# Performance work log

Hardware: AMD Instinct MI355X
Metric: run time of the kernel (lower is better)

The kernel has to match this reference:

```python
import jax, jax.numpy as jnp
import numpy as np

N = 50000   # nodes
K = 8       # fixed in-degree per node (edges sorted by target)
NQ = 400000 # quadruplets
TWO_PI = 2.0 * np.pi


def setup_inputs() -> dict:
    key = jax.random.key(0)
    k1, k2 = jax.random.split(key)
    pos = jax.random.normal(k1, (N, 3), dtype=jnp.float32) * 3.0
    # ring-structured graph: node i receives edges from (i+1..i+K) mod N.
    # Edges sorted by target i with exactly K per node -> edges into node n
    # occupy slots [n*K, n*K+K). Since N > 2K, a node is never its own
    # 2-hop self (idx_i != idx_k always holds, matching torch's mask).
    i = np.repeat(np.arange(N, dtype=np.int32), K)
    d = np.tile(np.arange(1, K + 1, dtype=np.int32), N)
    j = (i + d) % N
    edge_index = jnp.asarray(np.stack([j, i]), dtype=jnp.int32)  # [2, E]
    q_index = jax.random.randint(k2, (4, NQ), 0, N, dtype=jnp.int32)
    return {"pos": pos, "edge_index": edge_index, "q_index": q_index}


def _geometry(pos, edge_index, q_index):
    j, i = edge_index[0], edge_index[1]
    E = j.shape[0]

    rel = pos[i] - pos[j]
    dist = jnp.sqrt(jnp.sum(rel * rel, axis=-1))                 # [E]

    # ---- triplets: for edge e=(j->i), k ranges over in-neighbors of j ----
    ar = jnp.arange(K, dtype=j.dtype)
    idx_kj = (j[:, None] * K + ar[None, :]).reshape(-1)          # [T] edge ids k->j
    idx_ji = jnp.repeat(jnp.arange(E, dtype=j.dtype), K)         # [T] edge ids j->i
    idx_i = i[idx_ji]
    idx_j = j[idx_ji]
    idx_k = j[idx_kj]

    pos_ji = pos[idx_i] - pos[idx_j]                             # [T,3]
    pos_jk = pos[idx_k] - pos[idx_j]                             # [T,3]
    a = jnp.sum(pos_ji * pos_jk, axis=-1)
    b = jnp.linalg.norm(jnp.cross(pos_ji, pos_jk), axis=-1)
    angle = jnp.arctan2(b, a)                                    # [T]

    # ---- quadruplets: k_n ranges over the K in-neighbors of idx_j ----
    kn_edges = idx_j[:, None] * K + ar[None, :]                  # [T,K]
    idx_k_n = j[kn_edges]                                        # [T,K]
    pos_jkn = pos[idx_k_n] - pos[idx_j][:, None, :]              # [T,K,3]
    plane1 = jnp.cross(pos_ji, pos_jk)                           # [T,3]
    plane2 = jnp.cross(pos_ji[:, None, :], pos_jkn)              # [T,K,3]
    dist_ji = jnp.sqrt(jnp.sum(pos_ji * pos_ji, axis=-1))        # [T]
    a2 = jnp.sum(plane1[:, None, :] * plane2, axis=-1)           # [T,K]
    b2 = jnp.sum(jnp.cross(plane1[:, None, :], plane2) * pos_ji[:, None, :], axis=-1) / dist_ji[:, None]
    torsion = jnp.arctan2(b2, a2)
    torsion = jnp.where(torsion <= 0, torsion + TWO_PI, torsion)
    valid = (idx_k_n != idx_i[:, None]) & (idx_k_n != idx_k[:, None])
    # scatter_min over quadruplets grouped by triplet == masked row-min
    torsiona = jnp.min(jnp.where(valid, torsion, jnp.inf), axis=-1)  # [T]

    plane_s = 0.5 * jnp.sin(angle) * dist[idx_kj] * dist[idx_ji]     # [T]

    # ---- tetrahedron volumes for quadruplets q_index [4,NQ] ----
    pq = pos[q_index.T]                                          # [NQ,4,3]
    v1 = pq[:, 1] - pq[:, 0]
    v2 = pq[:, 2] - pq[:, 0]
    v3 = pq[:, 3] - pq[:, 0]
    volume = jnp.abs(jnp.sum(jnp.cross(v1, v2) * v3, axis=-1)) / 6.0  # [NQ]

    return dist, angle, torsiona, plane_s, volume, idx_ji, idx_kj


def reference(pos, edge_index, q_index):
    dist, angle, torsiona, plane_s, volume, idx_ji, idx_kj = _geometry(pos, edge_index, q_index)
    # matches torch return: (dist, angle, torsiona, torsiona, torsiona, plane_s, volume, idx_ji, idx_kj)
    return (dist, angle, torsiona, torsiona, torsiona, plane_s, volume, idx_ji, idx_kj)
```

## Files before the change

### kernel.cpp

```cpp
#include <hip/hip_runtime.h>

#define KDEG 8
constexpr float TWO_PI_F = 6.28318530717958647692f;
constexpr float PI_F = 3.14159265358979323846f;
constexpr float PI_2_F = 1.57079632679489661923f;
constexpr float MIN_SENTINEL = 1000.0f;

struct F3 { float x, y, z; };
__device__ __forceinline__ F3 f3sub(F3 a, F3 b) { return {a.x - b.x, a.y - b.y, a.z - b.z}; }
__device__ __forceinline__ float f3dot(F3 a, F3 b) { return a.x * b.x + a.y * b.y + a.z * b.z; }
__device__ __forceinline__ F3 f3cross(F3 a, F3 b) {
  return {a.y * b.z - a.z * b.y, a.z * b.x - a.x * b.z, a.x * b.y - a.y * b.x};
}
__device__ __forceinline__ F3 ldpos(const float* __restrict__ p, int idx) {
  return {p[3 * idx], p[3 * idx + 1], p[3 * idx + 2]};
}

__device__ __forceinline__ float fast_atan01(float z) {
  float z2 = z * z;
  float p = fmaf(z2, 0.0208351f, -0.0851330f);
  p = fmaf(z2, p, 0.1801410f);
  p = fmaf(z2, p, -0.3302995f);
  p = fmaf(z2, p, 0.9998660f);
  return z * p;
}

__device__ __forceinline__ float fast_atan2(float y, float x) {
  float ax = fabsf(x), ay = fabsf(y);
  float mx = fmaxf(ax, ay);
  float mn = fminf(ax, ay);
  float z = mn * __builtin_amdgcn_rcpf(fmaxf(mx, 1e-30f));
  float r = fast_atan01(z);
  r = (ay > ax) ? (PI_2_F - r) : r;
  r = (x < 0.0f) ? (PI_F - r) : r;
  return (y < 0.0f) ? -r : r;
}

__device__ __forceinline__ void edge_work(
    int e,
    const float* __restrict__ pos,
    const int* __restrict__ ei_j,
    const int* __restrict__ ei_i,
    float* __restrict__ out,
    int off_angle, int off_t0, int off_t1, int off_t2,
    int off_ps, int off_iji, int off_ikj)
{
  int j = ei_j[e];
  int i = ei_i[e];
  F3 pj = ldpos(pos, j);
  F3 pi = ldpos(pos, i);
  F3 pji = f3sub(pi, pj);
  float d2 = f3dot(pji, pji);
  float inv_dji = rsqrtf(d2);
  float dji = d2 * inv_dji;
  float inv_d2 = inv_dji * inv_dji;
  out[e] = dji;

  int base = j * KDEG;
  int nbr[KDEG];
#pragma unroll
  for (int n = 0; n < KDEG; n++) nbr[n] = ei_j[base + n];

  F3 u[KDEG], pl[KDEG];
  float s[KDEG], ang[KDEG], hb[KDEG];
#pragma unroll
  for (int n = 0; n < KDEG; n++) {
    u[n] = f3sub(ldpos(pos, nbr[n]), pj);
    s[n] = f3dot(pji, u[n]);
    pl[n] = f3cross(pji, u[n]);
    float b = sqrtf(f3dot(pl[n], pl[n]));
    ang[n] = fast_atan2(b, s[n]);
    hb[n] = 0.5f * b;
  }

  int t0 = e * KDEG;
  float4 v0, v1;
  v0 = {ang[0], ang[1], ang[2], ang[3]};
  v1 = {ang[4], ang[5], ang[6], ang[7]};
  *reinterpret_cast<float4*>(out + off_angle + t0) = v0;
  *reinterpret_cast<float4*>(out + off_angle + t0 + 4) = v1;
  v0 = {hb[0], hb[1], hb[2], hb[3]};
  v1 = {hb[4], hb[5], hb[6], hb[7]};
  *reinterpret_cast<float4*>(out + off_ps + t0) = v0;
  *reinterpret_cast<float4*>(out + off_ps + t0 + 4) = v1;

  bool vi[KDEG];
#pragma unroll
  for (int n = 0; n < KDEG; n++) vi[n] = (nbr[n] != i);

  float mn[KDEG];
#pragma unroll
  for (int n = 0; n < KDEG; n++) mn[n] = MIN_SENTINEL;

#pragma unroll
  for (int kk = 0; kk < KDEG; kk++) {
#pragma unroll
    for (int n = kk + 1; n < KDEG; n++) {
      float m = f3dot(u[kk], u[n]);
      float Traw = f3dot(u[kk], pl[n]);
      float x = fmaf(-s[kk] * s[n], inv_d2, m);
      float y = -Traw * inv_dji;
      float t1 = fast_atan2(y, x);
      float f1 = (t1 <= 0.0f) ? t1 + TWO_PI_F : t1;
      float t2 = -t1;
      float f2 = (t2 <= 0.0f) ? t2 + TWO_PI_F : t2;
      bool same = (nbr[n] == nbr[kk]);
      if (vi[n] && !same) mn[kk] = fminf(mn[kk], f1);
      if (vi[kk] && !same) mn[n] = fminf(mn[n], f2);
    }
  }

  v0 = {mn[0], mn[1], mn[2], mn[3]};
  v1 = {mn[4], mn[5], mn[6], mn[7]};
  *reinterpret_cast<float4*>(out + off_t0 + t0) = v0;
  *reinterpret_cast<float4*>(out + off_t0 + t0 + 4) = v1;
  *reinterpret_cast<float4*>(out + off_t1 + t0) = v0;
  *reinterpret_cast<float4*>(out + off_t1 + t0 + 4) = v1;
  *reinterpret_cast<float4*>(out + off_t2 + t0) = v0;
  *reinterpret_cast<float4*>(out + off_t2 + t0 + 4) = v1;

  float fe = (float)e;
  v0 = {fe, fe, fe, fe};
  *reinterpret_cast<float4*>(out + off_iji + t0) = v0;
  *reinterpret_cast<float4*>(out + off_iji + t0 + 4) = v0;

  float fb = (float)base;
  v0 = {fb, fb + 1.0f, fb + 2.0f, fb + 3.0f};
  v1 = {fb + 4.0f, fb + 5.0f, fb + 6.0f, fb + 7.0f};
  *reinterpret_cast<float4*>(out + off_ikj + t0) = v0;
  *reinterpret_cast<float4*>(out + off_ikj + t0 + 4) = v1;
}

__device__ __forceinline__ void volume_work(
    int t,
    const float* __restrict__ pos,
    const int* __restrict__ q,
    float* __restrict__ out,
    int NQ, int off_vol)
{
  int q0 = q[t];
  int q1 = q[t + NQ];
  int q2 = q[t + 2 * NQ];
  int q3 = q[t + 3 * NQ];
  F3 p0 = ldpos(pos, q0);
  F3 p1 = ldpos(pos, q1);
  F3 p2 = ldpos(pos, q2);
  F3 p3 = ldpos(pos, q3);
  F3 v1 = f3sub(p1, p0);
  F3 v2 = f3sub(p2, p0);
  F3 v3 = f3sub(p3, p0);
  float vol = fabsf(f3dot(f3cross(v1, v2), v3)) * (1.0f / 6.0f);
  out[off_vol + t] = vol;
}

__global__ __launch_bounds__(256) void fused_kernel(
    const float* __restrict__ pos,
    const int* __restrict__ ei_j,
    const int* __restrict__ ei_i,
    const int* __restrict__ q,
    float* __restrict__ out,
    int E, int NQ, int nbE,
    int off_angle, int off_t0, int off_t1, int off_t2,
    int off_ps, int off_vol, int off_iji, int off_ikj)
{
  int b = blockIdx.x;
  if (b < nbE) {
    int e = b * blockDim.x + threadIdx.x;
    if (e < E)
      edge_work(e, pos, ei_j, ei_i, out,
                off_angle, off_t0, off_t1, off_t2, off_ps, off_iji, off_ikj);
  } else {
    int t = (b - nbE) * blockDim.x + threadIdx.x;
    if (t < NQ)
      volume_work(t, pos, q, out, NQ, off_vol);
  }
}

extern "C" void kernel_launch(void* const* d_in, const int* in_sizes, int n_in,
                              void* d_out, int out_size, void* d_ws, size_t ws_size,
                              hipStream_t stream) {
  const float* pos = (const float*)d_in[0];
  const int* edge_index = (const int*)d_in[1];
  const int* q_index = (const int*)d_in[2];

  const int E = in_sizes[1] / 2;
  const int NQ = in_sizes[2] / 4;
  const int T = E * KDEG;

  const int* ei_j = edge_index;
  const int* ei_i = edge_index + E;

  float* out = (float*)d_out;

  const int off_angle = E;
  const int off_t0 = off_angle + T;
  const int off_t1 = off_t0 + T;
  const int off_t2 = off_t1 + T;
  const int off_ps = off_t2 + T;
  const int off_vol = off_ps + T;
  const int off_iji = off_vol + NQ;
  const int off_ikj = off_iji + T;
  (void)out_size; (void)d_ws; (void)ws_size; (void)n_in;

  const int blk = 256;
  const int nbE = (E + blk - 1) / blk;
  const int nbQ = (NQ + blk - 1) / blk;

  fused_kernel<<<nbE + nbQ, blk, 0, stream>>>(
      pos, ei_j, ei_i, q_index, out, E, NQ, nbE,
      off_angle, off_t0, off_t1, off_t2, off_ps, off_vol, off_iji, off_ikj);
}
```

Measured before the change: 33.21 us.

## Compute torsions as azimuth differences in a per-edge orthonormal frame

Builds a fixed perpendicular frame (e1, e2) around each edge direction and projects every neighbor onto it to get one azimuth per neighbor. The pairwise torsion angle then becomes a difference of two azimuths, which replaces the 28 atan2 calls plus dot and cross products in the inner pair loop with subtractions. Fewer live registers (no u/pl arrays) may also help occupancy. The risk is precision loss and wraparound near the ±pi edges of atan2, and a degenerate frame when the edge is parallel to the fixed vector G.

```diff
diff --git a/kernel.cpp b/kernel.cpp
--- a/kernel.cpp
+++ b/kernel.cpp
@@ -53,24 +53,32 @@
   float d2 = f3dot(pji, pji);
   float inv_dji = rsqrtf(d2);
   float dji = d2 * inv_dji;
-  float inv_d2 = inv_dji * inv_dji;
   out[e] = dji;
+
+  const F3 G = {0.53452248f, -0.26726124f, 0.80178373f};
+  F3 e1 = f3cross(pji, G);
+  F3 e2 = f3cross(pji, e1);
+  float L2 = f3dot(e1, e1);
+  float invL = rsqrtf(fmaxf(L2, 1e-30f));
+  float djinvL = dji * invL;
 
   int base = j * KDEG;
   int nbr[KDEG];
 #pragma unroll
   for (int n = 0; n < KDEG; n++) nbr[n] = ei_j[base + n];
 
-  F3 u[KDEG], pl[KDEG];
-  float s[KDEG], ang[KDEG], hb[KDEG];
+  float phi[KDEG], ang[KDEG], hb[KDEG];
 #pragma unroll
   for (int n = 0; n < KDEG; n++) {
-    u[n] = f3sub(ldpos(pos, nbr[n]), pj);
-    s[n] = f3dot(pji, u[n]);
-    pl[n] = f3cross(pji, u[n]);
-    float b = sqrtf(f3dot(pl[n], pl[n]));
-    ang[n] = fast_atan2(b, s[n]);
-    hb[n] = 0.5f * b;
+    F3 u = f3sub(ldpos(pos, nbr[n]), pj);
+    float s = f3dot(pji, u);
+    float a = f3dot(e1, u);
+    float b = f3dot(e2, u) * inv_dji;
+    phi[n] = fast_atan2(b, a);
+    float perp = sqrtf(fmaf(a, a, b * b));
+    float bfull = perp * djinvL;
+    ang[n] = fast_atan2(bfull, s);
+    hb[n] = 0.5f * bfull;
   }
 
   int t0 = e * KDEG;
@@ -84,6 +92,16 @@
   *reinterpret_cast<float4*>(out + off_ps + t0) = v0;
   *reinterpret_cast<float4*>(out + off_ps + t0 + 4) = v1;
 
+  float fe = (float)e;
+  v0 = {fe, fe, fe, fe};
+  *reinterpret_cast<float4*>(out + off_iji + t0) = v0;
+  *reinterpret_cast<float4*>(out + off_iji + t0 + 4) = v0;
+  float fb = (float)base;
+  v0 = {fb, fb + 1.0f, fb + 2.0f, fb + 3.0f};
+  v1 = {fb + 4.0f, fb + 5.0f, fb + 6.0f, fb + 7.0f};
+  *reinterpret_cast<float4*>(out + off_ikj + t0) = v0;
+  *reinterpret_cast<float4*>(out + off_ikj + t0 + 4) = v1;
+
   bool vi[KDEG];
 #pragma unroll
   for (int n = 0; n < KDEG; n++) vi[n] = (nbr[n] != i);
@@ -96,14 +114,10 @@
   for (int kk = 0; kk < KDEG; kk++) {
 #pragma unroll
     for (int n = kk + 1; n < KDEG; n++) {
-      float m = f3dot(u[kk], u[n]);
-      float Traw = f3dot(u[kk], pl[n]);
-      float x = fmaf(-s[kk] * s[n], inv_d2, m);
-      float y = -Traw * inv_dji;
-      float t1 = fast_atan2(y, x);
-      float f1 = (t1 <= 0.0f) ? t1 + TWO_PI_F : t1;
-      float t2 = -t1;
-      float f2 = (t2 <= 0.0f) ? t2 + TWO_PI_F : t2;
+      float d = phi[n] - phi[kk];
+      float f1 = (d <= 0.0f) ? d + TWO_PI_F : d;
+      float f2 = TWO_PI_F - f1;
+      f2 = (f2 <= 0.0f) ? f2 + TWO_PI_F : f2;
       bool same = (nbr[n] == nbr[kk]);
       if (vi[n] && !same) mn[kk] = fminf(mn[kk], f1);
       if (vi[kk] && !same) mn[n] = fminf(mn[n], f2);
@@ -118,17 +132,6 @@
   *reinterpret_cast<float4*>(out + off_t1 + t0 + 4) = v1;
   *reinterpret_cast<float4*>(out + off_t2 + t0) = v0;
   *reinterpret_cast<float4*>(out + off_t2 + t0 + 4) = v1;
-
-  float fe = (float)e;
-  v0 = {fe, fe, fe, fe};
-  *reinterpret_cast<float4*>(out + off_iji + t0) = v0;
-  *reinterpret_cast<float4*>(out + off_iji + t0 + 4) = v0;
-
-  float fb = (float)base;
-  v0 = {fb, fb + 1.0f, fb + 2.0f, fb + 3.0f};
-  v1 = {fb + 4.0f, fb + 5.0f, fb + 6.0f, fb + 7.0f};
-  *reinterpret_cast<float4*>(out + off_ikj + t0) = v0;
-  *reinterpret_cast<float4*>(out + off_ikj + t0 + 4) = v1;
 }
 
 __device__ __forceinline__ void volume_work(
```

After: 30.41 us (median of 2 runs). 1.09x faster.
